# Kernel optimization log

Hardware: AMD Instinct MI355X
Metric: run time of the kernel (lower is better)

The kernel has to match this reference:

```python
import jax, jax.numpy as jnp
import numpy as np

EPS = 1e-6
N_NODES = 50000
N_EDGES = 800000
IN_DIM = 128
OUT_DIM = 128
HEADS = 4
D_K = OUT_DIM // HEADS
ATT_DIM = 2 * D_K + 1  # use_edge_feat=True


def setup_inputs() -> dict:
    key = jax.random.key(0)
    ks = jax.random.split(key, 8)
    h = jax.random.normal(ks[0], (N_NODES, IN_DIM), dtype=jnp.float32)
    edge_index = jax.random.randint(ks[1], (2, N_EDGES), 0, N_NODES, dtype=jnp.int64)
    edge_feat = jax.random.normal(ks[2], (N_EDGES, 1), dtype=jnp.float32)
    # parameters
    W_w = jax.random.normal(ks[3], (OUT_DIM, IN_DIM), dtype=jnp.float32) / np.sqrt(IN_DIM)
    W_b = jnp.zeros((OUT_DIM,), dtype=jnp.float32)
    att = jax.random.normal(ks[4], (HEADS, ATT_DIM), dtype=jnp.float32)
    ln_g = jnp.ones((OUT_DIM,), dtype=jnp.float32)
    ln_b = jnp.zeros((OUT_DIM,), dtype=jnp.float32)
    return {"h": h, "edge_index": edge_index, "edge_feat": edge_feat,
            "W_w": W_w, "W_b": W_b, "att": att, "ln_g": ln_g, "ln_b": ln_b}


def _layer_norm(x, g, b):
    mu = jnp.mean(x, axis=-1, keepdims=True)
    var = jnp.mean(jnp.square(x - mu), axis=-1, keepdims=True)
    return (x - mu) * jax.lax.rsqrt(var + 1e-5) * g + b


def reference(h, edge_index, edge_feat, W_w, W_b, att, ln_g, ln_b):
    num_nodes = h.shape[0]
    z = h @ W_w.T + W_b                      # [N, out_dim]
    zr = z.reshape(num_nodes, HEADS, D_K)    # [N, H, d_k]
    src, dst = edge_index[0], edge_index[1]
    h_s = zr[src]                            # [E, H, d_k]
    h_d = zr[dst]                            # [E, H, d_k]
    f_e = jnp.broadcast_to(edge_feat[:, None, :], (edge_feat.shape[0], HEADS, 1))
    concat = jnp.concatenate([h_s, h_d, f_e], axis=-1)  # [E, H, att_dim]
    scores = jnp.sum(concat * att[None], axis=-1)        # [E, H]
    scores = jnp.where(scores >= 0, scores, 0.2 * scores)  # LeakyReLU(0.2)
    scores = jnp.clip(scores, -20.0, 20.0)
    alpha = jnp.exp(scores)                               # [E, H]
    denom = jax.ops.segment_sum(alpha, dst, num_segments=num_nodes)  # [N, H]
    norm_alpha = alpha / (denom[dst] + EPS)               # [E, H]
    weighted = h_s * norm_alpha[..., None]                # [E, H, d_k]
    out = jax.ops.segment_sum(weighted, dst, num_segments=num_nodes)  # [N, H, d_k]
    out = out.reshape(num_nodes, OUT_DIM) + z
    out = _layer_norm(out, ln_g, ln_b)
    return jax.nn.elu(out)
```

## Files before the change

### kernel.cpp

```cpp
#include <hip/hip_runtime.h>
#include <hip/hip_bf16.h>
#include <math.h>

typedef __attribute__((ext_vector_type(8))) short bf16x8;
typedef __attribute__((ext_vector_type(4))) float f32x4;

__device__ __forceinline__ unsigned short f2bf(float f) {
    unsigned u = __float_as_uint(f);
    unsigned r = ((u >> 16) & 1u) + 0x7fffu;
    return (unsigned short)((u + r) >> 16);
}
__device__ __forceinline__ float bfL(unsigned u) { return __uint_as_float(u << 16); }
__device__ __forceinline__ float bfH(unsigned u) { return __uint_as_float(u & 0xffff0000u); }

#define SCORE_NPB 32

__global__ __launch_bounds__(256) void k_prep(const float* __restrict__ W,
                                              const float* __restrict__ bias,
                                              const float* __restrict__ att,
                                              const float* __restrict__ h,
                                              unsigned short* __restrict__ Wb16,
                                              float* __restrict__ s_src,
                                              float* __restrict__ s_dst,
                                              int* __restrict__ head4,
                                              int N, int scoreBlocks) {
    const int t = threadIdx.x;
    const int bid = blockIdx.x;
    if (bid == 0) {
#pragma unroll
        for (int q = 0; q < 8; ++q) {
            int gi = q * 256 + t;
            int kg = gi >> 7, row = gi & 127;
            int kbase = (kg >> 2) * 32 + (kg & 3) * 4;
            unsigned pk[4];
#pragma unroll
            for (int p = 0; p < 4; ++p) {
                int e0 = 2 * p, e1 = 2 * p + 1;
                float v0 = W[(size_t)row * 128 + kbase + (e0 >> 2) * 16 + (e0 & 3)];
                float v1 = W[(size_t)row * 128 + kbase + (e1 >> 2) * 16 + (e1 & 3)];
                pk[p] = ((unsigned)f2bf(v1) << 16) | f2bf(v0);
            }
            *reinterpret_cast<uint4*>(&Wb16[(size_t)gi * 8]) =
                make_uint4(pk[0], pk[1], pk[2], pk[3]);
        }
    } else if (bid <= scoreBlocks) {
        __shared__ float wsdL[2][4][128];
        __shared__ float cs[8];
#pragma unroll
        for (int q = 0; q < 4; ++q) {
            int idx = q * 256 + t;
            int isD = idx >> 9, rem = idx & 511;
            int hd = rem >> 7, k = rem & 127;
            float w = 0.f;
            for (int j = 0; j < 32; ++j)
                w += W[(size_t)(hd * 32 + j) * 128 + k] * att[hd * 65 + isD * 32 + j];
            wsdL[isD][hd][k] = w;
        }
        if (t < 8) {
            int chd = t & 3, cIsD = t >> 2;
            float c = 0.f;
            for (int j = 0; j < 32; ++j)
                c += bias[chd * 32 + j] * att[chd * 65 + cIsD * 32 + j];
            cs[t] = c;
        }
        __syncthreads();
        int node = (bid - 1) * SCORE_NPB + (t >> 3);
        int p = t & 7;
        if (node < N) {
            const float* hp = h + (size_t)node * 128 + p * 16;
            float ss[4] = {0.f, 0.f, 0.f, 0.f}, sd[4] = {0.f, 0.f, 0.f, 0.f};
#pragma unroll
            for (int q = 0; q < 4; ++q) {
                float4 hv = *reinterpret_cast<const float4*>(hp + q * 4);
#pragma unroll
                for (int hd = 0; hd < 4; ++hd) {
                    const float* wa = &wsdL[0][hd][p * 16 + q * 4];
                    const float* wb = &wsdL[1][hd][p * 16 + q * 4];
                    ss[hd] += hv.x * wa[0] + hv.y * wa[1] + hv.z * wa[2] + hv.w * wa[3];
                    sd[hd] += hv.x * wb[0] + hv.y * wb[1] + hv.z * wb[2] + hv.w * wb[3];
                }
            }
#pragma unroll
            for (int off = 1; off < 8; off <<= 1)
#pragma unroll
                for (int hd = 0; hd < 4; ++hd) {
                    ss[hd] += __shfl_xor(ss[hd], off);
                    sd[hd] += __shfl_xor(sd[hd], off);
                }
            if (p == 0) {
                *reinterpret_cast<float4*>(&s_src[(size_t)node * 4]) =
                    make_float4(ss[0] + cs[0], ss[1] + cs[1], ss[2] + cs[2], ss[3] + cs[3]);
                *reinterpret_cast<float4*>(&s_dst[(size_t)node * 4]) =
                    make_float4(sd[0] + cs[4], sd[1] + cs[5], sd[2] + cs[6], sd[3] + cs[7]);
            }
        }
    } else {
        int i = ((bid - 1 - scoreBlocks) * 256 + t) * 4;
        if (i < N * 4)
            *reinterpret_cast<int4*>(&head4[i]) = make_int4(-1, -1, -1, -1);
    }
}

__global__ __launch_bounds__(256) void k_work(
        const float* __restrict__ h, const unsigned short* __restrict__ Wb16,
        const float* __restrict__ bias, unsigned short* __restrict__ zb16,
        const int* __restrict__ src, const int* __restrict__ dst,
        const float* __restrict__ ef, const float* __restrict__ att,
        const float* __restrict__ s_src, const float* __restrict__ s_dst,
        int* __restrict__ head4, int4* __restrict__ epkt,
        int N, int E, int gemmBlocks) {
    __shared__ short hS[16 * 64 * 8];
    const int t = threadIdx.x;
    const int bid = blockIdx.x;

    if (bid >= gemmBlocks) {
        int e = (bid - gemmBlocks) * 256 + t;
        if (e >= E) return;
        int s = src[e], d = dst[e];
        float fv = ef[e];
        float4 ss = *reinterpret_cast<const float4*>(&s_src[(size_t)s * 4]);
        float4 sd = *reinterpret_cast<const float4*>(&s_dst[(size_t)d * 4]);
        float aE0 = att[64], aE1 = att[129], aE2 = att[194], aE3 = att[259];
        float sc0 = ss.x + sd.x + fv * aE0;
        float sc1 = ss.y + sd.y + fv * aE1;
        float sc2 = ss.z + sd.z + fv * aE2;
        float sc3 = ss.w + sd.w + fv * aE3;
        sc0 = sc0 >= 0.f ? sc0 : 0.2f * sc0;  sc1 = sc1 >= 0.f ? sc1 : 0.2f * sc1;
        sc2 = sc2 >= 0.f ? sc2 : 0.2f * sc2;  sc3 = sc3 >= 0.f ? sc3 : 0.2f * sc3;
        float a0 = expf(fminf(fmaxf(sc0, -20.f), 20.f));
        float a1 = expf(fminf(fmaxf(sc1, -20.f), 20.f));
        float a2 = expf(fminf(fmaxf(sc2, -20.f), 20.f));
        float a3 = expf(fminf(fmaxf(sc3, -20.f), 20.f));
        int prev = atomicExch(&head4[(size_t)d * 4 + (e & 3)], e);
        epkt[e] = make_int4(s, prev,
            (int)(((unsigned)f2bf(a1) << 16) | f2bf(a0)),
            (int)(((unsigned)f2bf(a3) << 16) | f2bf(a2)));
        return;
    }

    const int by = bid & 1;
    const int n0 = (bid >> 1) * 64;
    const int obase = by * 64;
#pragma unroll
    for (int q = 0; q < 8; ++q) {
        int f = q * 256 + t;
        int nd = f >> 5;
        int k4 = (f & 31) * 4;
        int ks = k4 >> 5, rr = k4 & 31;
        int half = rr >> 4, g = (rr & 15) >> 2;
        int kg = ks * 4 + g;
        int slot = kg * 64 + (nd ^ (kg & 7));
        int hn = n0 + nd; if (hn > N - 1) hn = N - 1;
        float4 v = *reinterpret_cast<const float4*>(&h[(size_t)hn * 128 + k4]);
        uint2 pk = make_uint2(((unsigned)f2bf(v.y) << 16) | f2bf(v.x),
                              ((unsigned)f2bf(v.w) << 16) | f2bf(v.z));
        *reinterpret_cast<uint2*>(&hS[slot * 8 + half * 4]) = pk;
    }
    __syncthreads();

    const int wv = t >> 6, l = t & 63;
    const int la = l & 15, lb = l >> 4;
    const int nbase = wv * 16;
    const int node = n0 + nbase + la;

    bf16x8 hfr[4];
#pragma unroll
    for (int ks = 0; ks < 4; ++ks) {
        int kg = ks * 4 + lb;
        int slot = kg * 64 + ((nbase + la) ^ (kg & 7));
        hfr[ks] = *reinterpret_cast<const bf16x8*>(&hS[slot * 8]);
    }

#pragma unroll
    for (int ot = 0; ot < 4; ++ot) {
        f32x4 acc = {0.f, 0.f, 0.f, 0.f};
#pragma unroll
        for (int ks = 0; ks < 4; ++ks) {
            int kg = ks * 4 + lb;
            bf16x8 wfr = *reinterpret_cast<const bf16x8*>(
                &Wb16[((size_t)kg * 128 + obase + ot * 16 + la) * 8]);
            acc = __builtin_amdgcn_mfma_f32_16x16x32_bf16(wfr, hfr[ks], acc, 0, 0, 0);
        }
        int colb = obase + ot * 16 + lb * 4;
        float4 bq = *reinterpret_cast<const float4*>(&bias[colb]);
        if (node < N) {
            uint2 pk = make_uint2(
                ((unsigned)f2bf(acc[1] + bq.y) << 16) | f2bf(acc[0] + bq.x),
                ((unsigned)f2bf(acc[3] + bq.w) << 16) | f2bf(acc[2] + bq.z));
            *reinterpret_cast<uint2*>(&zb16[(size_t)node * 128 + colb]) = pk;
        }
    }
}

__global__ __launch_bounds__(256) void k_agg_final(const int* __restrict__ head4,
                                                   const int4* __restrict__ epkt,
                                                   const uint4* __restrict__ zb4,
                                                   const float* __restrict__ g,
                                                   const float* __restrict__ bparm,
                                                   float* __restrict__ out, int N) {
    int wave = threadIdx.x >> 6, lane = threadIdx.x & 63;
    int l8 = lane & 7;
    int n = blockIdx.x * 32 + wave * 8 + (lane >> 3);
    if (n >= N) return;
    const int hd = l8 >> 1;
    int4 eh = *reinterpret_cast<const int4*>(&head4[(size_t)n * 4]);
    int e0 = eh.x, e1 = eh.y, e2 = eh.z, e3 = eh.w;
    float X0 = 0.f, X1 = 0.f, X2 = 0.f, X3 = 0.f;
    float X4 = 0.f, X5 = 0.f, X6 = 0.f, X7 = 0.f;
    float X8 = 0.f, X9 = 0.f, Xa = 0.f, Xb = 0.f;
    float Xc = 0.f, Xd = 0.f, Xe = 0.f, Xf = 0.f;
    float da = 0.f;
#define UNPK(P, AV) { unsigned u = (hd & 2) ? (unsigned)(P).w : (unsigned)(P).z; \
    AV = (hd & 1) ? bfH(u) : bfL(u); }
#define STEP(EV) if (EV != -1) { \
        int4 p = epkt[EV]; \
        uint4 q0 = zb4[(size_t)p.x * 16 + l8 * 2]; \
        uint4 q1 = zb4[(size_t)p.x * 16 + l8 * 2 + 1]; \
        float a; UNPK(p, a) \
        X0 += bfL(q0.x) * a; X1 += bfH(q0.x) * a; \
        X2 += bfL(q0.y) * a; X3 += bfH(q0.y) * a; \
        X4 += bfL(q0.z) * a; X5 += bfH(q0.z) * a; \
        X6 += bfL(q0.w) * a; X7 += bfH(q0.w) * a; \
        X8 += bfL(q1.x) * a; X9 += bfH(q1.x) * a; \
        Xa += bfL(q1.y) * a; Xb += bfH(q1.y) * a; \
        Xc += bfL(q1.z) * a; Xd += bfH(q1.z) * a; \
        Xe += bfL(q1.w) * a; Xf += bfH(q1.w) * a; \
        da += a; EV = p.y; }
    while (((e0 & e1) & (e2 & e3)) != -1) {
        STEP(e0) STEP(e1) STEP(e2) STEP(e3)
    }
#undef STEP
#undef UNPK

    float inv = 1.f / (da + 1e-6f);
    uint4 qz0 = zb4[(size_t)n * 16 + l8 * 2];
    uint4 qz1 = zb4[(size_t)n * 16 + l8 * 2 + 1];
    float x0 = X0 * inv + bfL(qz0.x), x1 = X1 * inv + bfH(qz0.x);
    float x2 = X2 * inv + bfL(qz0.y), x3 = X3 * inv + bfH(qz0.y);
    float x4 = X4 * inv + bfL(qz0.z), x5 = X5 * inv + bfH(qz0.z);
    float x6 = X6 * inv + bfL(qz0.w), x7 = X7 * inv + bfH(qz0.w);
    float x8 = X8 * inv + bfL(qz1.x), x9 = X9 * inv + bfH(qz1.x);
    float xa = Xa * inv + bfL(qz1.y), xb = Xb * inv + bfH(qz1.y);
    float xc = Xc * inv + bfL(qz1.z), xd = Xd * inv + bfH(qz1.z);
    float xe = Xe * inv + bfL(qz1.w), xf = Xf * inv + bfH(qz1.w);
    float s = (((x0 + x1) + (x2 + x3)) + ((x4 + x5) + (x6 + x7)))
            + (((x8 + x9) + (xa + xb)) + ((xc + xd) + (xe + xf)));
#pragma unroll
    for (int off = 1; off < 8; off <<= 1) s += __shfl_xor(s, off);
    float mu = s * (1.f / 128.f);
    float d0 = x0 - mu, d1 = x1 - mu, d2 = x2 - mu, d3 = x3 - mu;
    float d4 = x4 - mu, d5 = x5 - mu, d6 = x6 - mu, d7 = x7 - mu;
    float d8 = x8 - mu, d9 = x9 - mu, dA = xa - mu, dB = xb - mu;
    float dC = xc - mu, dD = xd - mu, dE = xe - mu, dF = xf - mu;
    float q = (((d0 * d0 + d1 * d1) + (d2 * d2 + d3 * d3))
             + ((d4 * d4 + d5 * d5) + (d6 * d6 + d7 * d7)))
            + (((d8 * d8 + d9 * d9) + (dA * dA + dB * dB))
             + ((dC * dC + dD * dD) + (dE * dE + dF * dF)));
#pragma unroll
    for (int off = 1; off < 8; off <<= 1) q += __shfl_xor(q, off);
    float rstd = rsqrtf(q * (1.f / 128.f) + 1e-5f);
    const int c = l8 * 16;
    float dv[16] = {d0, d1, d2, d3, d4, d5, d6, d7, d8, d9, dA, dB, dC, dD, dE, dF};
#pragma unroll
    for (int qb = 0; qb < 4; ++qb) {
        float4 gg = *reinterpret_cast<const float4*>(&g[c + qb * 4]);
        float4 bb = *reinterpret_cast<const float4*>(&bparm[c + qb * 4]);
        float y0 = dv[qb * 4 + 0] * rstd * gg.x + bb.x;
        float y1 = dv[qb * 4 + 1] * rstd * gg.y + bb.y;
        float y2 = dv[qb * 4 + 2] * rstd * gg.z + bb.z;
        float y3 = dv[qb * 4 + 3] * rstd * gg.w + bb.w;
        y0 = y0 > 0.f ? y0 : expf(y0) - 1.f;
        y1 = y1 > 0.f ? y1 : expf(y1) - 1.f;
        y2 = y2 > 0.f ? y2 : expf(y2) - 1.f;
        y3 = y3 > 0.f ? y3 : expf(y3) - 1.f;
        *reinterpret_cast<float4*>(&out[(size_t)n * 128 + c + qb * 4]) =
            make_float4(y0, y1, y2, y3);
    }
}

extern "C" void kernel_launch(void* const* d_in, const int* in_sizes, int n_in,
                              void* d_out, int out_size, void* d_ws, size_t ws_size,
                              hipStream_t stream) {
    const float* h   = (const float*)d_in[0];
    const int*   ei  = (const int*)d_in[1];
    const float* ef  = (const float*)d_in[2];
    const float* Ww  = (const float*)d_in[3];
    const float* Wb  = (const float*)d_in[4];
    const float* att = (const float*)d_in[5];
    const float* lng = (const float*)d_in[6];
    const float* lnb = (const float*)d_in[7];
    float* out = (float*)d_out;

    const int N = in_sizes[0] / 128;
    const int E = in_sizes[1] / 2;
    const int* src = ei;
    const int* dst = ei + E;

    char* ws = (char*)d_ws;
    unsigned short* zb16   = (unsigned short*)ws; ws += (size_t)N * 128 * 2;
    unsigned short* Wb16   = (unsigned short*)ws; ws += (size_t)128 * 128 * 2;
    float*          s_src  = (float*)ws;          ws += (size_t)N * 4 * 4;
    float*          s_dst  = (float*)ws;          ws += (size_t)N * 4 * 4;
    int*            head4  = (int*)ws;            ws += (size_t)N * 4 * 4;
    int4*           epkt   = (int4*)ws;           ws += (size_t)E * 16;

    const int scoreBlocks = (N + SCORE_NPB - 1) / SCORE_NPB;
    const int headBlocks  = (N + 255) / 256;
    k_prep<<<1 + scoreBlocks + headBlocks, 256, 0, stream>>>(
        Ww, Wb, att, h, Wb16, s_src, s_dst, head4, N, scoreBlocks);

    const int gemmBlocks = ((N + 63) / 64) * 2;
    const int edgeBlocks = (E + 255) / 256;
    k_work<<<gemmBlocks + edgeBlocks, 256, 0, stream>>>(
        h, Wb16, Wb, zb16, src, dst, ef, att, s_src, s_dst, head4, epkt,
        N, E, gemmBlocks);
    k_agg_final<<<(N + 31) / 32, 256, 0, stream>>>(head4, epkt,
                                                   (const uint4*)zb16, lng, lnb, out, N);
}
```

Baseline: 116.7 us.

## Use eight per-node edge lists balanced by atomic counter for aggregation

Result: slower. 145.5 us (+24.7%).

```diff
diff --git a/kernel.cpp b/kernel.cpp
--- a/kernel.cpp
+++ b/kernel.cpp
@@ -13,7 +13,7 @@
 __device__ __forceinline__ float bfL(unsigned u) { return __uint_as_float(u << 16); }
 __device__ __forceinline__ float bfH(unsigned u) { return __uint_as_float(u & 0xffff0000u); }
 
-#define SCORE_NPB 32
+#define SCORE_NPB 128
 
 __global__ __launch_bounds__(256) void k_prep(const float* __restrict__ W,
                                               const float* __restrict__ bias,
@@ -22,8 +22,9 @@
                                               unsigned short* __restrict__ Wb16,
                                               float* __restrict__ s_src,
                                               float* __restrict__ s_dst,
-                                              int* __restrict__ head4,
-                                              int N, int scoreBlocks) {
+                                              int* __restrict__ head8,
+                                              int* __restrict__ cnt,
+                                              int N, int scoreBlocks, int headBlocks) {
     const int t = threadIdx.x;
     const int bid = blockIdx.x;
     if (bid == 0) {
@@ -64,9 +65,11 @@
             cs[t] = c;
         }
         __syncthreads();
-        int node = (bid - 1) * SCORE_NPB + (t >> 3);
-        int p = t & 7;
-        if (node < N) {
+        const int p = t & 7;
+#pragma unroll
+        for (int it = 0; it < 4; ++it) {
+            int node = (bid - 1) * SCORE_NPB + it * 32 + (t >> 3);
+            if (node >= N) continue;
             const float* hp = h + (size_t)node * 128 + p * 16;
             float ss[4] = {0.f, 0.f, 0.f, 0.f}, sd[4] = {0.f, 0.f, 0.f, 0.f};
 #pragma unroll
@@ -94,10 +97,14 @@
                     make_float4(sd[0] + cs[4], sd[1] + cs[5], sd[2] + cs[6], sd[3] + cs[7]);
             }
         }
+    } else if (bid <= scoreBlocks + headBlocks) {
+        int i = ((bid - 1 - scoreBlocks) * 256 + t) * 4;
+        if (i < N * 8)
+            *reinterpret_cast<int4*>(&head8[i]) = make_int4(-1, -1, -1, -1);
     } else {
-        int i = ((bid - 1 - scoreBlocks) * 256 + t) * 4;
-        if (i < N * 4)
-            *reinterpret_cast<int4*>(&head4[i]) = make_int4(-1, -1, -1, -1);
+        int i = ((bid - 1 - scoreBlocks - headBlocks) * 256 + t) * 4;
+        if (i < N)
+            *reinterpret_cast<int4*>(&cnt[i]) = make_int4(0, 0, 0, 0);
     }
 }
 
@@ -107,7 +114,7 @@
         const int* __restrict__ src, const int* __restrict__ dst,
         const float* __restrict__ ef, const float* __restrict__ att,
         const float* __restrict__ s_src, const float* __restrict__ s_dst,
-        int* __restrict__ head4, int4* __restrict__ epkt,
+        int* __restrict__ head8, int* __restrict__ cnt, int4* __restrict__ epkt,
         int N, int E, int gemmBlocks) {
     __shared__ short hS[16 * 64 * 8];
     const int t = threadIdx.x;
@@ -131,7 +138,8 @@
         float a1 = expf(fminf(fmaxf(sc1, -20.f), 20.f));
         float a2 = expf(fminf(fmaxf(sc2, -20.f), 20.f));
         float a3 = expf(fminf(fmaxf(sc3, -20.f), 20.f));
-        int prev = atomicExch(&head4[(size_t)d * 4 + (e & 3)], e);
+        int ci = atomicAdd(&cnt[d], 1) & 7;
+        int prev = atomicExch(&head8[(size_t)d * 8 + ci], e);
         epkt[e] = make_int4(s, prev,
             (int)(((unsigned)f2bf(a1) << 16) | f2bf(a0)),
             (int)(((unsigned)f2bf(a3) << 16) | f2bf(a2)));
@@ -192,7 +200,7 @@
     }
 }
 
-__global__ __launch_bounds__(256) void k_agg_final(const int* __restrict__ head4,
+__global__ __launch_bounds__(256) void k_agg_final(const int* __restrict__ head8,
                                                    const int4* __restrict__ epkt,
                                                    const uint4* __restrict__ zb4,
                                                    const float* __restrict__ g,
@@ -203,8 +211,10 @@
     int n = blockIdx.x * 32 + wave * 8 + (lane >> 3);
     if (n >= N) return;
     const int hd = l8 >> 1;
-    int4 eh = *reinterpret_cast<const int4*>(&head4[(size_t)n * 4]);
-    int e0 = eh.x, e1 = eh.y, e2 = eh.z, e3 = eh.w;
+    int4 eha = *reinterpret_cast<const int4*>(&head8[(size_t)n * 8]);
+    int4 ehb = *reinterpret_cast<const int4*>(&head8[(size_t)n * 8 + 4]);
+    int e0 = eha.x, e1 = eha.y, e2 = eha.z, e3 = eha.w;
+    int e4 = ehb.x, e5 = ehb.y, e6 = ehb.z, e7 = ehb.w;
     float X0 = 0.f, X1 = 0.f, X2 = 0.f, X3 = 0.f;
     float X4 = 0.f, X5 = 0.f, X6 = 0.f, X7 = 0.f;
     float X8 = 0.f, X9 = 0.f, Xa = 0.f, Xb = 0.f;
@@ -226,8 +236,9 @@
         Xc += bfL(q1.z) * a; Xd += bfH(q1.z) * a; \
         Xe += bfL(q1.w) * a; Xf += bfH(q1.w) * a; \
         da += a; EV = p.y; }
-    while (((e0 & e1) & (e2 & e3)) != -1) {
+    while ((((e0 & e1) & (e2 & e3)) & ((e4 & e5) & (e6 & e7))) != -1) {
         STEP(e0) STEP(e1) STEP(e2) STEP(e3)
+        STEP(e4) STEP(e5) STEP(e6) STEP(e7)
     }
 #undef STEP
 #undef UNPK
@@ -301,19 +312,21 @@
     unsigned short* Wb16   = (unsigned short*)ws; ws += (size_t)128 * 128 * 2;
     float*          s_src  = (float*)ws;          ws += (size_t)N * 4 * 4;
     float*          s_dst  = (float*)ws;          ws += (size_t)N * 4 * 4;
-    int*            head4  = (int*)ws;            ws += (size_t)N * 4 * 4;
+    int*            head8  = (int*)ws;            ws += (size_t)N * 8 * 4;
+    int*            cnt    = (int*)ws;            ws += (size_t)N * 4;
     int4*           epkt   = (int4*)ws;           ws += (size_t)E * 16;
 
     const int scoreBlocks = (N + SCORE_NPB - 1) / SCORE_NPB;
-    const int headBlocks  = (N + 255) / 256;
-    k_prep<<<1 + scoreBlocks + headBlocks, 256, 0, stream>>>(
-        Ww, Wb, att, h, Wb16, s_src, s_dst, head4, N, scoreBlocks);
+    const int headBlocks  = (N * 8 / 4 + 255) / 256;
+    const int cntBlocks   = (N / 4 + 255) / 256;
+    k_prep<<<1 + scoreBlocks + headBlocks + cntBlocks, 256, 0, stream>>>(
+        Ww, Wb, att, h, Wb16, s_src, s_dst, head8, cnt, N, scoreBlocks, headBlocks);
 
     const int gemmBlocks = ((N + 63) / 64) * 2;
     const int edgeBlocks = (E + 255) / 256;
     k_work<<<gemmBlocks + edgeBlocks, 256, 0, stream>>>(
-        h, Wb16, Wb, zb16, src, dst, ef, att, s_src, s_dst, head4, epkt,
+        h, Wb16, Wb, zb16, src, dst, ef, att, s_src, s_dst, head8, cnt, epkt,
         N, E, gemmBlocks);
-    k_agg_final<<<(N + 31) / 32, 256, 0, stream>>>(head4, epkt,
+    k_agg_final<<<(N + 31) / 32, 256, 0, stream>>>(head8, epkt,
                                                    (const uint4*)zb16, lng, lnb, out, N);
 }
```
